# Performance work log

Measured on AMD Instinct MI355X. Metric: run time of the kernel, lower is better.

Reference implementation:

```python
import jax, jax.numpy as jnp
import numpy as np

N = 16_777_216
P = 100  # number of percentile bins


def setup_inputs() -> dict:
    key = jax.random.key(0)
    k1, k2 = jax.random.split(key)
    outputs = jax.random.uniform(k1, (N,), dtype=jnp.float32)
    targets = jax.random.uniform(k2, (N,), dtype=jnp.float32)
    percentiles = jnp.linspace(0.01, 1.0, P, dtype=jnp.float32)
    return {"outputs": outputs, "targets": targets, "percentiles": percentiles}


def _nearest_bin(percentiles, targets):
    # Equivalent to argmin(|percentiles - t|) for sorted percentiles,
    # with ties broken toward the lower index (matching torch.argmin).
    j = jnp.searchsorted(percentiles, targets)          # insertion point in [0, P]
    jl = jnp.clip(j - 1, 0, percentiles.shape[0] - 1)
    jr = jnp.clip(j, 0, percentiles.shape[0] - 1)
    dl = jnp.abs(percentiles[jl] - targets)
    dr = jnp.abs(percentiles[jr] - targets)
    return jnp.where(dl <= dr, jl, jr)


def reference(outputs, targets, percentiles):
    max_bin = percentiles.shape[0]
    idx = _nearest_bin(percentiles, targets)            # int32 [N]
    factors = (idx.astype(outputs.dtype) + 1.0) / max_bin
    errors = targets - outputs
    losses = jnp.maximum((factors - 1.0) * errors, factors * errors)
    return jnp.mean(losses)
```

## Files before the change

### kernel.cpp

```cpp
#include <hip/hip_runtime.h>

#define THREADS 256
#define GRID 2048
#define UNROLL 4

__global__ __launch_bounds__(THREADS) void loss_partial_kernel(
    const float* __restrict__ outputs,
    const float* __restrict__ targets,
    const float* __restrict__ per,
    float* __restrict__ partials,
    int n, int P, float inv_maxbin) {

    const float p0 = per[0];
    const float pL = per[P - 1];
    const float inv_h = (float)(P - 1) / (pL - p0);
    const float kmax = (float)(P - 1);

    const int n4 = n >> 2;
    const float4* __restrict__ o4 = (const float4*)outputs;
    const float4* __restrict__ t4 = (const float4*)targets;

    const int tid = blockIdx.x * THREADS + threadIdx.x;
    const int stride = GRID * THREADS;

    float acc = 0.0f;

    int i = tid;

    for (; i + (UNROLL - 1) * stride < n4; i += UNROLL * stride) {
        float4 o[UNROLL], t[UNROLL];
        #pragma unroll
        for (int u = 0; u < UNROLL; ++u) {
            o[u] = o4[i + u * stride];
            t[u] = t4[i + u * stride];
        }
        #pragma unroll
        for (int u = 0; u < UNROLL; ++u) {
            #pragma unroll
            for (int c = 0; c < 4; ++c) {
                float tv = (c == 0) ? t[u].x : (c == 1) ? t[u].y : (c == 2) ? t[u].z : t[u].w;
                float ov = (c == 0) ? o[u].x : (c == 1) ? o[u].y : (c == 2) ? o[u].z : o[u].w;
                float k = rintf((tv - p0) * inv_h);
                k = fminf(fmaxf(k, 0.0f), kmax);
                float f = (k + 1.0f) * inv_maxbin;
                float e = tv - ov;
                acc += fmaxf((f - 1.0f) * e, f * e);
            }
        }
    }

    for (; i < n4; i += stride) {
        float4 o = o4[i];
        float4 t = t4[i];
        #pragma unroll
        for (int c = 0; c < 4; ++c) {
            float tv = (c == 0) ? t.x : (c == 1) ? t.y : (c == 2) ? t.z : t.w;
            float ov = (c == 0) ? o.x : (c == 1) ? o.y : (c == 2) ? o.z : o.w;
            float k = rintf((tv - p0) * inv_h);
            k = fminf(fmaxf(k, 0.0f), kmax);
            float f = (k + 1.0f) * inv_maxbin;
            float e = tv - ov;
            acc += fmaxf((f - 1.0f) * e, f * e);
        }
    }

    const int tail = n & 3;
    if (tail && blockIdx.x == 0 && threadIdx.x < tail) {
        int j = (n4 << 2) + threadIdx.x;
        float tv = targets[j];
        float ov = outputs[j];
        float k = rintf((tv - p0) * inv_h);
        k = fminf(fmaxf(k, 0.0f), kmax);
        float f = (k + 1.0f) * inv_maxbin;
        float e = tv - ov;
        acc += fmaxf((f - 1.0f) * e, f * e);
    }

    #pragma unroll
    for (int off = 32; off > 0; off >>= 1)
        acc += __shfl_down(acc, off, 64);

    __shared__ float lds[THREADS / 64];
    const int lane = threadIdx.x & 63;
    const int wave = threadIdx.x >> 6;
    if (lane == 0) lds[wave] = acc;
    __syncthreads();
    if (threadIdx.x == 0) {
        float s = 0.0f;
        #pragma unroll
        for (int w = 0; w < THREADS / 64; ++w) s += lds[w];
        partials[blockIdx.x] = s;
    }
}

__global__ __launch_bounds__(THREADS) void finalize_kernel(
    const float* __restrict__ partials, int nblocks,
    float* __restrict__ out, double inv_n) {

    double acc = 0.0;
    for (int i = threadIdx.x; i < nblocks; i += blockDim.x)
        acc += (double)partials[i];

    #pragma unroll
    for (int off = 32; off > 0; off >>= 1)
        acc += __shfl_down(acc, off, 64);

    __shared__ double lds[THREADS / 64];
    const int lane = threadIdx.x & 63;
    const int wave = threadIdx.x >> 6;
    if (lane == 0) lds[wave] = acc;
    __syncthreads();
    if (threadIdx.x == 0) {
        double s = 0.0;
        #pragma unroll
        for (int w = 0; w < THREADS / 64; ++w) s += lds[w];
        out[0] = (float)(s * inv_n);
    }
}

extern "C" void kernel_launch(void* const* d_in, const int* in_sizes, int n_in,
                              void* d_out, int out_size, void* d_ws, size_t ws_size,
                              hipStream_t stream) {
    const float* outputs     = (const float*)d_in[0];
    const float* targets     = (const float*)d_in[1];
    const float* percentiles = (const float*)d_in[2];
    float* out = (float*)d_out;

    const int n = in_sizes[0];
    const int P = in_sizes[2];

    float* partials = (float*)d_ws;

    loss_partial_kernel<<<GRID, THREADS, 0, stream>>>(
        outputs, targets, percentiles, partials, n, P, 1.0f / (float)P);

    finalize_kernel<<<1, THREADS, 0, stream>>>(
        partials, GRID, out, 1.0 / (double)n);
}
```

Baseline: 149.2 us.

## Fuse finalize into main kernel via last-block atomic counter and deepen loads

Replaces the separate finalize kernel with a last-block-done pattern: each block release-stores its partial and bumps an atomic counter, and the final block reduces all partials in double. The per-thread unroll rises from 4 to 8 float4 pairs, with the loads grouped and a sched_barrier placed before compute. A hipMemsetAsync resets the counter each call, which still leaves a small operation ahead of the kernel. The goal is to drop one kernel launch and raise memory-level parallelism, at the cost of more registers and atomic traffic.

```diff
diff --git a/kernel.cpp b/kernel.cpp
--- a/kernel.cpp
+++ b/kernel.cpp
@@ -2,14 +2,16 @@
 
 #define THREADS 256
 #define GRID 2048
-#define UNROLL 4
+#define PT 8
 
-__global__ __launch_bounds__(THREADS) void loss_partial_kernel(
+__global__ __launch_bounds__(THREADS) void loss_kernel(
     const float* __restrict__ outputs,
     const float* __restrict__ targets,
     const float* __restrict__ per,
     float* __restrict__ partials,
-    int n, int P, float inv_maxbin) {
+    unsigned int* __restrict__ cnt,
+    float* __restrict__ out,
+    int n, int P, float inv_maxbin, double inv_n) {
 
     const float p0 = per[0];
     const float pL = per[P - 1];
@@ -21,21 +23,20 @@
     const float4* __restrict__ t4 = (const float4*)targets;
 
     const int tid = blockIdx.x * THREADS + threadIdx.x;
-    const int stride = GRID * THREADS;
+    const int S = GRID * THREADS;
 
     float acc = 0.0f;
-
     int i = tid;
 
-    for (; i + (UNROLL - 1) * stride < n4; i += UNROLL * stride) {
-        float4 o[UNROLL], t[UNROLL];
+    for (; i + (PT - 1) * S < n4; i += PT * S) {
+        float4 o[PT], t[PT];
         #pragma unroll
-        for (int u = 0; u < UNROLL; ++u) {
-            o[u] = o4[i + u * stride];
-            t[u] = t4[i + u * stride];
-        }
+        for (int u = 0; u < PT; ++u) o[u] = o4[i + u * S];
         #pragma unroll
-        for (int u = 0; u < UNROLL; ++u) {
+        for (int u = 0; u < PT; ++u) t[u] = t4[i + u * S];
+        __builtin_amdgcn_sched_barrier(0);
+        #pragma unroll
+        for (int u = 0; u < PT; ++u) {
             #pragma unroll
             for (int c = 0; c < 4; ++c) {
                 float tv = (c == 0) ? t[u].x : (c == 1) ? t[u].y : (c == 2) ? t[u].z : t[u].w;
@@ -49,7 +50,7 @@
         }
     }
 
-    for (; i < n4; i += stride) {
+    for (; i < n4; i += S) {
         float4 o = o4[i];
         float4 t = t4[i];
         #pragma unroll
@@ -81,40 +82,42 @@
         acc += __shfl_down(acc, off, 64);
 
     __shared__ float lds[THREADS / 64];
+    __shared__ int is_last;
     const int lane = threadIdx.x & 63;
     const int wave = threadIdx.x >> 6;
     if (lane == 0) lds[wave] = acc;
     __syncthreads();
+
     if (threadIdx.x == 0) {
         float s = 0.0f;
         #pragma unroll
         for (int w = 0; w < THREADS / 64; ++w) s += lds[w];
-        partials[blockIdx.x] = s;
+        __hip_atomic_store(&partials[blockIdx.x], s, __ATOMIC_RELEASE,
+                           __HIP_MEMORY_SCOPE_AGENT);
+        unsigned int old = __hip_atomic_fetch_add(cnt, 1u, __ATOMIC_ACQ_REL,
+                                                  __HIP_MEMORY_SCOPE_AGENT);
+        is_last = (old == (unsigned int)(gridDim.x - 1)) ? 1 : 0;
     }
-}
+    __syncthreads();
 
-__global__ __launch_bounds__(THREADS) void finalize_kernel(
-    const float* __restrict__ partials, int nblocks,
-    float* __restrict__ out, double inv_n) {
+    if (is_last) {
+        double a = 0.0;
+        for (int j = threadIdx.x; j < (int)gridDim.x; j += THREADS)
+            a += (double)__hip_atomic_load(&partials[j], __ATOMIC_RELAXED,
+                                           __HIP_MEMORY_SCOPE_AGENT);
+        #pragma unroll
+        for (int off = 32; off > 0; off >>= 1)
+            a += __shfl_down(a, off, 64);
 
-    double acc = 0.0;
-    for (int i = threadIdx.x; i < nblocks; i += blockDim.x)
-        acc += (double)partials[i];
-
-    #pragma unroll
-    for (int off = 32; off > 0; off >>= 1)
-        acc += __shfl_down(acc, off, 64);
-
-    __shared__ double lds[THREADS / 64];
-    const int lane = threadIdx.x & 63;
-    const int wave = threadIdx.x >> 6;
-    if (lane == 0) lds[wave] = acc;
-    __syncthreads();
-    if (threadIdx.x == 0) {
-        double s = 0.0;
-        #pragma unroll
-        for (int w = 0; w < THREADS / 64; ++w) s += lds[w];
-        out[0] = (float)(s * inv_n);
+        __shared__ double dlds[THREADS / 64];
+        if (lane == 0) dlds[wave] = a;
+        __syncthreads();
+        if (threadIdx.x == 0) {
+            double sd = 0.0;
+            #pragma unroll
+            for (int w = 0; w < THREADS / 64; ++w) sd += dlds[w];
+            out[0] = (float)(sd * inv_n);
+        }
     }
 }
 
@@ -130,10 +133,11 @@
     const int P = in_sizes[2];
 
     float* partials = (float*)d_ws;
+    unsigned int* cnt = (unsigned int*)((char*)d_ws + GRID * sizeof(float));
 
-    loss_partial_kernel<<<GRID, THREADS, 0, stream>>>(
-        outputs, targets, percentiles, partials, n, P, 1.0f / (float)P);
+    hipMemsetAsync(cnt, 0, sizeof(unsigned int), stream);
 
-    finalize_kernel<<<1, THREADS, 0, stream>>>(
-        partials, GRID, out, 1.0 / (double)n);
+    loss_kernel<<<GRID, THREADS, 0, stream>>>(
+        outputs, targets, percentiles, partials, cnt, out,
+        n, P, 1.0f / (float)P, 1.0 / (double)n);
 }
```

Result: slower. 327.3 us (+119.4%).
